# Kernel tuning notes

Measured on AMD Instinct MI355X. Metric: run time of the kernel, lower is better.

Reference implementation:

```python
import jax, jax.numpy as jnp
import numpy as np

B, L, H, E, F, C = 8, 8192, 512, 8, 1024, 2  # batch, seq, hidden, experts, ffn, capacity factor


def setup_inputs() -> dict:
    key = jax.random.key(0)
    ks = jax.random.split(key, 4)
    x = jax.random.normal(ks[0], (B, L, H), jnp.float32)
    Wg = jax.random.normal(ks[1], (H, E), jnp.float32) * (H ** -0.5)   # gate (no bias)
    W1 = jax.random.normal(ks[2], (E, H, F), jnp.float32) * (H ** -0.5)
    b1 = jnp.zeros((E, F), jnp.float32)
    W2 = jax.random.normal(ks[3], (E, F, H), jnp.float32) * (F ** -0.5)
    b2 = jnp.zeros((E, H), jnp.float32)
    return {"x": x, "Wg": Wg, "W1": W1, "b1": b1, "W2": W2, "b2": b2}


def reference(x, Wg, W1, b1, W2, b2):
    b, l, h = x.shape
    e = Wg.shape[1]
    k = min(max(int(l * C / e), 1), l)  # expert-choice capacity per expert
    # Gate scores: softmax over experts per token, then each expert picks its top-k tokens.
    S = jax.nn.softmax(x @ Wg, axis=-1)          # (b, l, E)
    St = jnp.swapaxes(S, 1, 2)                   # (b, E, l)
    G, I = jax.lax.top_k(St, k)                  # (b, E, k) scores / token indices
    # Dispatch: gather each expert's chosen tokens.
    ex = jnp.take_along_axis(x[:, None], I[..., None], axis=2)   # (b, E, k, h)
    # Grouped expert MLP (Linear -> GELU -> Linear), batched over experts.
    hmid = jax.nn.gelu(jnp.einsum('bekh,ehf->bekf', ex, W1) + b1[None, :, None, :],
                       approximate=False)
    out = jnp.einsum('bekf,efh->bekh', hmid, W2) + b2[None, :, None, :]
    vals = G[..., None] * out                    # weight by gate score
    # Combine: scatter-add expert outputs back to token positions.
    new_x = jnp.zeros_like(x).at[jnp.arange(b)[:, None, None], I].add(vals)
    return new_x
```

## Files before the change

kernel.cpp:

```cpp
#include <hip/hip_runtime.h>
#include <hip/hip_bf16.h>
#include <hip/hip_fp16.h>

typedef float f32x4 __attribute__((ext_vector_type(4)));
typedef _Float16 f16x8 __attribute__((ext_vector_type(8)));

static constexpr int Bb = 8, Ll = 8192, Hh = 512, Ee = 8, Ff = 1024, KK = 2048;

static __device__ __forceinline__ float fast_rcp(float x) {
#if __has_builtin(__builtin_amdgcn_rcpf)
  return __builtin_amdgcn_rcpf(x);
#else
  return 1.0f / x;
#endif
}

static __device__ __forceinline__ float gelu_exact(float v) {
  float a = __builtin_fabsf(v) * 0.70710678118654752f;
  float t = fast_rcp(__builtin_fmaf(0.3275911f, a, 1.0f));
  float p = __builtin_fmaf(1.061405429f, t, -1.453152027f);
  p = __builtin_fmaf(p, t, 1.421413741f);
  p = __builtin_fmaf(p, t, -0.284496736f);
  p = __builtin_fmaf(p, t, 0.254829592f);
  p = p * t;
  float e = __expf(-a * a);
  float er = __builtin_fmaf(-p, e, 1.0f);
  er = __builtin_copysignf(er, v);
  return 0.5f * v * (1.0f + er);
}

__global__ __launch_bounds__(256) void cvt_f16_kernel(const float* __restrict__ src,
                                                      _Float16* __restrict__ dst, int n4) {
  int i = blockIdx.x * blockDim.x + threadIdx.x;
  int stride = gridDim.x * blockDim.x;
  for (; i < n4; i += stride) {
    float4 v = reinterpret_cast<const float4*>(src)[i];
    union { _Float16 h[4]; uint2 u; } cv;
    cv.h[0] = (_Float16)v.x; cv.h[1] = (_Float16)v.y;
    cv.h[2] = (_Float16)v.z; cv.h[3] = (_Float16)v.w;
    reinterpret_cast<uint2*>(dst)[i] = cv.u;
  }
}

__global__ __launch_bounds__(256) void transpose_cvt_kernel(const float* __restrict__ src,
                                                            _Float16* __restrict__ dst,
                                                            int R, int C) {
  __shared__ float tile[32][33];
  int z = blockIdx.z;
  const float* s = src + (size_t)z * R * C;
  _Float16* d = dst + (size_t)z * R * C;
  int c0 = blockIdx.x * 32, r0 = blockIdx.y * 32;
  int tx = threadIdx.x, ty = threadIdx.y;
#pragma unroll
  for (int i = ty; i < 32; i += 8) tile[i][tx] = s[(size_t)(r0 + i) * C + (c0 + tx)];
  __syncthreads();
#pragma unroll
  for (int i = ty; i < 32; i += 8) d[(size_t)(c0 + i) * R + (r0 + tx)] = (_Float16)tile[tx][i];
}

__global__ __launch_bounds__(256) void gate_kernel(const float* __restrict__ x,
                                                   const float* __restrict__ Wg,
                                                   double* __restrict__ St) {
  __shared__ float wgt[8][516];
  __shared__ float xs[32][68];
  int tid = threadIdx.x;
  for (int i = tid; i < Hh * Ee; i += 256) {
    int h = i >> 3, e = i & 7;
    wgt[e][h] = Wg[i];
  }
  int tl = tid >> 3, e = tid & 7;
  int token0 = blockIdx.x * 32;
  double acc = 0.0;
  for (int c = 0; c < 8; ++c) {
    __syncthreads();
#pragma unroll
    for (int i = tid; i < 512; i += 256) {
      int row = i >> 4, c4 = i & 15;
      float4 v = reinterpret_cast<const float4*>(x + (size_t)(token0 + row) * Hh + c * 64)[c4];
      *reinterpret_cast<float4*>(&xs[row][c4 * 4]) = v;
    }
    __syncthreads();
#pragma unroll
    for (int h = 0; h < 64; h += 4) {
      float4 xv = *reinterpret_cast<const float4*>(&xs[tl][h]);
      float4 wv = *reinterpret_cast<const float4*>(&wgt[e][c * 64 + h]);
      acc += (double)xv.x * (double)wv.x;
      acc += (double)xv.y * (double)wv.y;
      acc += (double)xv.z * (double)wv.z;
      acc += (double)xv.w * (double)wv.w;
    }
  }
  double m = acc;
  m = fmax(m, __shfl_xor(m, 1, 64));
  m = fmax(m, __shfl_xor(m, 2, 64));
  m = fmax(m, __shfl_xor(m, 4, 64));
  double ex = exp(acc - m);
  double s = ex;
  s += __shfl_xor(s, 1, 64);
  s += __shfl_xor(s, 2, 64);
  s += __shfl_xor(s, 4, 64);
  int token = token0 + tl;
  int b = token >> 13, l = token & (Ll - 1);
  St[((size_t)(b * Ee + e)) * Ll + l] = ex / s;
}

__global__ __launch_bounds__(1024) void topk_kernel(const double* __restrict__ St,
                                                    int* __restrict__ idx,
                                                    float* __restrict__ gate) {
  __shared__ unsigned long long keys[Ll];
  __shared__ unsigned int hist[256];
  __shared__ unsigned int sc[1024];
  __shared__ unsigned long long s_prefix;
  __shared__ int s_remaining;
  __shared__ unsigned long long redA[16], redO[16];
  int row = blockIdx.x;
  int tid = threadIdx.x;
  const double* s = St + (size_t)row * Ll;
  unsigned long long myA = ~0ULL, myO = 0ULL;
  for (int i = tid; i < Ll; i += 1024) {
    unsigned long long kx = (unsigned long long)__double_as_longlong(s[i]);
    keys[i] = kx;
    myA &= kx;
    myO |= kx;
  }
#pragma unroll
  for (int off2 = 32; off2 >= 1; off2 >>= 1) {
    myA &= __shfl_xor(myA, off2, 64);
    myO |= __shfl_xor(myO, off2, 64);
  }
  if ((tid & 63) == 0) { redA[tid >> 6] = myA; redO[tid >> 6] = myO; }
  __syncthreads();
  unsigned long long allA = redA[0], allO = redO[0];
#pragma unroll
  for (int w = 1; w < 16; ++w) { allA &= redA[w]; allO |= redO[w]; }
  unsigned long long diff = allA ^ allO;

  unsigned long long T;
  int nEqTake;
  if (diff == 0) {
    T = allA;
    nEqTake = KK;
  } else {
    int hb = 63 - __builtin_clzll(diff);
    int pv = hb >> 3;
    unsigned long long prefmask = (pv >= 7) ? 0ULL : (~0ULL << ((pv + 1) * 8));
    unsigned long long prefix = allA & prefmask;
    int remaining = KK;
    for (int p = pv; p >= 0; --p) {
      if (tid < 256) hist[tid] = 0;
      __syncthreads();
      int sh = p * 8;
      for (int i = tid; i < Ll; i += 1024) {
        unsigned long long kk = keys[i];
        if ((kk & prefmask) == prefix) atomicAdd(&hist[(unsigned)(kk >> sh) & 255u], 1u);
      }
      __syncthreads();
      if (tid < 256) sc[tid] = hist[tid];
      __syncthreads();
#pragma unroll
      for (int off = 1; off < 256; off <<= 1) {
        unsigned v = (tid < 256 && tid + off < 256) ? sc[tid + off] : 0;
        __syncthreads();
        if (tid < 256) sc[tid] += v;
        __syncthreads();
      }
      if (tid < 256) {
        unsigned incl = sc[tid];
        unsigned above = (tid == 255) ? 0u : sc[tid + 1];
        if ((int)incl >= remaining && (int)above < remaining) {
          s_remaining = remaining - (int)above;
          s_prefix = prefix | ((unsigned long long)(unsigned)tid << sh);
        }
      }
      __syncthreads();
      remaining = s_remaining;
      prefix = s_prefix;
      prefmask |= (255ULL << sh);
      __syncthreads();
    }
    T = prefix;
    nEqTake = remaining;
  }

  int base = tid * 8;
  unsigned long long kk[8];
  unsigned gtc = 0, eqc = 0;
#pragma unroll
  for (int j = 0; j < 8; ++j) {
    kk[j] = keys[base + j];
    gtc += (kk[j] > T);
    eqc += (kk[j] == T);
  }
  unsigned packed = (gtc << 16) | eqc;
  sc[tid] = packed;
  __syncthreads();
  for (int off = 1; off < 1024; off <<= 1) {
    unsigned v = (tid >= off) ? sc[tid - off] : 0;
    __syncthreads();
    sc[tid] += v;
    __syncthreads();
  }
  unsigned excl = sc[tid] - packed;
  int gtb = (int)(excl >> 16), eqb = (int)(excl & 0xFFFFu);
  int orow = row * KK;
#pragma unroll
  for (int j = 0; j < 8; ++j) {
    bool isgt = kk[j] > T, iseq = kk[j] == T;
    bool take = isgt || (iseq && eqb < nEqTake);
    if (take) {
      int pos = gtb + (eqb < nEqTake ? eqb : nEqTake);
      idx[orow + pos] = base + j;
      gate[orow + pos] = (float)__longlong_as_double((long long)kk[j]);
    }
    gtb += isgt ? 1 : 0;
    eqb += iseq ? 1 : 0;
  }
}

__global__ __launch_bounds__(256) void buildinv_kernel(const int* __restrict__ idx,
                                                       int* __restrict__ cnt,
                                                       int* __restrict__ inv) {
  int s = blockIdx.x * 256 + threadIdx.x;
  int gp = s >> 11;
  int b = gp >> 3;
  int t = idx[s];
  int key = b * Ll + t;
  int pos = atomicAdd(&cnt[key], 1);
  inv[key * 8 + pos] = s;
}

__global__ __launch_bounds__(256) void combine_kernel(const _Float16* __restrict__ yout,
                                                      const int* __restrict__ cnt,
                                                      const int* __restrict__ inv,
                                                      float* __restrict__ out) {
  int tglob = blockIdx.x * 4 + (threadIdx.x >> 6);
  int lane = threadIdx.x & 63;
  int n = cnt[tglob];
  float acc[8];
#pragma unroll
  for (int j = 0; j < 8; ++j) acc[j] = 0.f;
  for (int c = 0; c < n; ++c) {
    int s = inv[tglob * 8 + c];
    f16x8 v = *reinterpret_cast<const f16x8*>(yout + (size_t)s * Hh + lane * 8);
#pragma unroll
    for (int j = 0; j < 8; ++j) acc[j] += (float)v[j];
  }
  float* o = out + (size_t)tglob * Hh + lane * 8;
  f32x4 lo = {acc[0], acc[1], acc[2], acc[3]};
  f32x4 hi = {acc[4], acc[5], acc[6], acc[7]};
  *reinterpret_cast<f32x4*>(o) = lo;
  *reinterpret_cast<f32x4*>(o + 4) = hi;
}

__global__ __launch_bounds__(512, 2) void gemm1_kernel(const _Float16* __restrict__ xb,
                                                       const _Float16* __restrict__ w1t,
                                                       const float* __restrict__ b1,
                                                       const int* __restrict__ idx,
                                                       _Float16* __restrict__ hmid,
                                                       int chunk_base) {
  __shared__ __align__(16) _Float16 lds[65536];
  int tid = threadIdx.x, lane = tid & 63, wid = tid >> 6;
  int gp = chunk_base + blockIdx.z;
  int b = gp >> 3, e = gp & 7;
  int m0 = blockIdx.y * 256, f0 = blockIdx.x * 256;

  const _Float16* srcbase[4];
  int dstoff[4];
#pragma unroll
  for (int i = 0; i < 4; ++i) {
    int c = wid * 4 + i;
    int lr = (c & 15) * 16 + (lane >> 2);
    int q = lane & 3;
    int qg = q ^ ((lr >> 1) & 3);
    if (c < 16) {
      int token = idx[(size_t)gp * KK + m0 + lr];
      srcbase[i] = xb + ((size_t)b * Ll + token) * Hh + qg * 8;
      dstoff[i] = (c & 15) * 512;
    } else {
      srcbase[i] = w1t + ((size_t)e * Ff + f0 + lr) * Hh + qg * 8;
      dstoff[i] = 8192 + (c & 15) * 512;
    }
  }

  f32x4 acc[8][4] = {};
  int wm = wid >> 2, wn = wid & 3;
  int a_off[8], b_off[4];
  int ko = lane >> 4;
#pragma unroll
  for (int i = 0; i < 8; ++i) {
    int ra = wm * 128 + i * 16 + (lane & 15);
    a_off[i] = ra * 32 + (ko ^ ((ra >> 1) & 3)) * 8;
  }
#pragma unroll
  for (int i = 0; i < 4; ++i) {
    int rb = wn * 64 + i * 16 + (lane & 15);
    b_off[i] = 8192 + rb * 32 + (ko ^ ((rb >> 1) & 3)) * 8;
  }

  auto stage = [&](int p, int kt) {
#pragma unroll
    for (int i = 0; i < 4; ++i) {
      __builtin_amdgcn_global_load_lds(
          (const __attribute__((address_space(1))) void*)(srcbase[i] + kt),
          (__attribute__((address_space(3))) void*)(lds + p * 16384 + dstoff[i]), 16, 0, 0);
    }
  };

  constexpr int nt = Hh / 32;
  stage(0, 0);
  stage(1, 32);
  for (int t = 0; t < nt; ++t) {
    __builtin_amdgcn_sched_barrier(0);
    if (t + 1 < nt) asm volatile("s_waitcnt vmcnt(4) lgkmcnt(0)" ::: "memory");
    else            asm volatile("s_waitcnt vmcnt(0) lgkmcnt(0)" ::: "memory");
    __builtin_amdgcn_s_barrier();
    __builtin_amdgcn_sched_barrier(0);
    if (t + 2 < nt) stage((t + 2) & 3, (t + 2) * 32);
    const _Float16* buf = lds + (t & 3) * 16384;
    f16x8 af[8], bf[4];
#pragma unroll
    for (int i = 0; i < 8; ++i) af[i] = *reinterpret_cast<const f16x8*>(buf + a_off[i]);
#pragma unroll
    for (int i = 0; i < 4; ++i) bf[i] = *reinterpret_cast<const f16x8*>(buf + b_off[i]);
    __builtin_amdgcn_s_setprio(1);
#pragma unroll
    for (int fr = 0; fr < 8; ++fr)
#pragma unroll
      for (int fc = 0; fc < 4; ++fc)
        acc[fr][fc] = __builtin_amdgcn_mfma_f32_16x16x32_f16(af[fr], bf[fc], acc[fr][fc], 0, 0, 0);
    __builtin_amdgcn_s_setprio(0);
  }
  __syncthreads();

  int cidx = lane & 15, rbase = (lane >> 4) * 4;
  float b1v[4];
#pragma unroll
  for (int fc = 0; fc < 4; ++fc) b1v[fc] = b1[e * Ff + f0 + wn * 64 + fc * 16 + cidx];
#pragma unroll
  for (int fr = 0; fr < 8; ++fr) {
#pragma unroll
    for (int fc = 0; fc < 4; ++fc) {
#pragma unroll
      for (int r = 0; r < 4; ++r) {
        int lm = wm * 128 + fr * 16 + rbase + r;
        int lf = wn * 64 + fc * 16 + cidx;
        float v = acc[fr][fc][r] + b1v[fc];
        float g = gelu_exact(v);
        lds[lm * 256 + (((lf >> 3) ^ (lm & 7)) << 3) + (lf & 7)] = (_Float16)g;
      }
    }
  }
  __syncthreads();
  _Float16* hd = hmid + (size_t)blockIdx.z * KK * Ff;
  int orow = tid >> 5, seg = tid & 31;
#pragma unroll
  for (int pp = 0; pp < 16; ++pp) {
    int lm = pp * 16 + orow;
    f16x8 v = *reinterpret_cast<const f16x8*>(lds + lm * 256 + ((seg ^ (lm & 7)) << 3));
    *reinterpret_cast<f16x8*>(hd + (size_t)(m0 + lm) * Ff + f0 + seg * 8) = v;
  }
}

__global__ __launch_bounds__(512, 2) void gemm2_kernel(const _Float16* __restrict__ hmid,
                                                       const _Float16* __restrict__ w2t,
                                                       const float* __restrict__ b2,
                                                       const int* __restrict__ idx,
                                                       const float* __restrict__ gate,
                                                       _Float16* __restrict__ yout,
                                                       int chunk_base) {
  __shared__ __align__(16) _Float16 lds[65536];
  int tid = threadIdx.x, lane = tid & 63, wid = tid >> 6;
  int gp = chunk_base + blockIdx.z;
  int e = gp & 7;
  int m0 = blockIdx.y * 256, h0 = blockIdx.x * 256;

  const _Float16* srcbase[4];
  int dstoff[4];
#pragma unroll
  for (int i = 0; i < 4; ++i) {
    int c = wid * 4 + i;
    int lr = (c & 15) * 16 + (lane >> 2);
    int q = lane & 3;
    int qg = q ^ ((lr >> 1) & 3);
    if (c < 16) {
      srcbase[i] = hmid + ((size_t)blockIdx.z * KK + m0 + lr) * Ff + qg * 8;
      dstoff[i] = (c & 15) * 512;
    } else {
      srcbase[i] = w2t + ((size_t)e * Hh + h0 + lr) * Ff + qg * 8;
      dstoff[i] = 8192 + (c & 15) * 512;
    }
  }

  f32x4 acc[8][4] = {};
  int wm = wid >> 2, wn = wid & 3;
  int a_off[8], b_off[4];
  int ko = lane >> 4;
#pragma unroll
  for (int i = 0; i < 8; ++i) {
    int ra = wm * 128 + i * 16 + (lane & 15);
    a_off[i] = ra * 32 + (ko ^ ((ra >> 1) & 3)) * 8;
  }
#pragma unroll
  for (int i = 0; i < 4; ++i) {
    int rb = wn * 64 + i * 16 + (lane & 15);
    b_off[i] = 8192 + rb * 32 + (ko ^ ((rb >> 1) & 3)) * 8;
  }

  auto stage = [&](int p, int kt) {
#pragma unroll
    for (int i = 0; i < 4; ++i) {
      __builtin_amdgcn_global_load_lds(
          (const __attribute__((address_space(1))) void*)(srcbase[i] + kt),
          (__attribute__((address_space(3))) void*)(lds + p * 16384 + dstoff[i]), 16, 0, 0);
    }
  };

  constexpr int nt = Ff / 32;
  stage(0, 0);
  stage(1, 32);
  for (int t = 0; t < nt; ++t) {
    __builtin_amdgcn_sched_barrier(0);
    if (t + 1 < nt) asm volatile("s_waitcnt vmcnt(4) lgkmcnt(0)" ::: "memory");
    else            asm volatile("s_waitcnt vmcnt(0) lgkmcnt(0)" ::: "memory");
    __builtin_amdgcn_s_barrier();
    __builtin_amdgcn_sched_barrier(0);
    if (t + 2 < nt) stage((t + 2) & 3, (t + 2) * 32);
    const _Float16* buf = lds + (t & 3) * 16384;
    f16x8 af[8], bf[4];
#pragma unroll
    for (int i = 0; i < 8; ++i) af[i] = *reinterpret_cast<const f16x8*>(buf + a_off[i]);
#pragma unroll
    for (int i = 0; i < 4; ++i) bf[i] = *reinterpret_cast<const f16x8*>(buf + b_off[i]);
    __builtin_amdgcn_s_setprio(1);
#pragma unroll
    for (int fr = 0; fr < 8; ++fr)
#pragma unroll
      for (int fc = 0; fc < 4; ++fc)
        acc[fr][fc] = __builtin_amdgcn_mfma_f32_16x16x32_f16(af[fr], bf[fc], acc[fr][fc], 0, 0, 0);
    __builtin_amdgcn_s_setprio(0);
  }
  __syncthreads();

  int cidx = lane & 15, rbase = (lane >> 4) * 4;
  float b2v[4];
#pragma unroll
  for (int fc = 0; fc < 4; ++fc) b2v[fc] = b2[e * Hh + h0 + wn * 64 + fc * 16 + cidx];
#pragma unroll
  for (int fr = 0; fr < 8; ++fr) {
    float gv[4];
#pragma unroll
    for (int r = 0; r < 4; ++r) {
      int lm = wm * 128 + fr * 16 + rbase + r;
      gv[r] = gate[(size_t)gp * KK + m0 + lm];
    }
#pragma unroll
    for (int fc = 0; fc < 4; ++fc) {
#pragma unroll
      for (int r = 0; r < 4; ++r) {
        int lm = wm * 128 + fr * 16 + rbase + r;
        int lh = wn * 64 + fc * 16 + cidx;
        float v = acc[fr][fc][r] + b2v[fc];
        lds[lm * 256 + (((lh >> 3) ^ (lm & 7)) << 3) + (lh & 7)] = (_Float16)(gv[r] * v);
      }
    }
  }
  __syncthreads();
  int orow = tid >> 5, seg = tid & 31;
#pragma unroll
  for (int pp = 0; pp < 16; ++pp) {
    int lm = pp * 16 + orow;
    f16x8 v = *reinterpret_cast<const f16x8*>(lds + lm * 256 + ((seg ^ (lm & 7)) << 3));
    *reinterpret_cast<f16x8*>(yout + ((size_t)gp * KK + m0 + lm) * Hh + h0 + seg * 8) = v;
  }
}

extern "C" void kernel_launch(void* const* d_in, const int* in_sizes, int n_in,
                              void* d_out, int out_size, void* d_ws, size_t ws_size,
                              hipStream_t stream) {
  const float* x  = (const float*)d_in[0];
  const float* Wg = (const float*)d_in[1];
  const float* W1 = (const float*)d_in[2];
  const float* b1 = (const float*)d_in[3];
  const float* W2 = (const float*)d_in[4];
  const float* b2 = (const float*)d_in[5];
  float* out = (float*)d_out;

  char* ws = (char*)d_ws;
  size_t off = 0;
  auto alloc = [&](size_t bytes) -> char* {
    char* p = ws + off;
    off = (off + bytes + 255) & ~(size_t)255;
    return p;
  };
  _Float16* xb   = (_Float16*)alloc((size_t)Bb * Ll * Hh * 2);
  _Float16* w1t  = (_Float16*)alloc((size_t)Ee * Ff * Hh * 2);
  _Float16* w2t  = (_Float16*)alloc((size_t)Ee * Hh * Ff * 2);
  double*   St   = (double*)alloc((size_t)Bb * Ee * Ll * 8);
  int*      dI   = (int*)alloc((size_t)Bb * Ee * KK * 4);
  float*    dG   = (float*)alloc((size_t)Bb * Ee * KK * 4);
  int*      cnt  = (int*)alloc((size_t)Bb * Ll * 4);
  int*      inv  = (int*)alloc((size_t)Bb * Ll * 8 * 4);
  _Float16* yout = (_Float16*)alloc((size_t)Bb * Ee * KK * Hh * 2);
  size_t fixed = off;
  size_t per_pair = (size_t)KK * Ff * 2;
  int chunk = 1;
  if (fixed + per_pair * 16 <= ws_size) chunk = 16;
  else if (fixed + per_pair * 8 <= ws_size) chunk = 8;
  else if (fixed + per_pair * 4 <= ws_size) chunk = 4;
  else if (fixed + per_pair * 2 <= ws_size) chunk = 2;
  _Float16* hmid = (_Float16*)alloc(per_pair * (size_t)chunk);

  hipMemsetAsync(cnt, 0, (size_t)Bb * Ll * 4, stream);
  cvt_f16_kernel<<<4096, 256, 0, stream>>>(x, xb, Bb * Ll * Hh / 4);
  transpose_cvt_kernel<<<dim3(Ff / 32, Hh / 32, Ee), dim3(32, 8), 0, stream>>>(W1, w1t, Hh, Ff);
  transpose_cvt_kernel<<<dim3(Hh / 32, Ff / 32, Ee), dim3(32, 8), 0, stream>>>(W2, w2t, Ff, Hh);
  gate_kernel<<<Bb * Ll / 32, 256, 0, stream>>>(x, Wg, St);
  topk_kernel<<<Bb * Ee, 1024, 0, stream>>>(St, dI, dG);
  buildinv_kernel<<<Bb * Ee * KK / 256, 256, 0, stream>>>(dI, cnt, inv);

  for (int cb = 0; cb < Bb * Ee; cb += chunk) {
    gemm1_kernel<<<dim3(Ff / 256, KK / 256, chunk), 512, 0, stream>>>(xb, w1t, b1, dI, hmid, cb);
    gemm2_kernel<<<dim3(Hh / 256, KK / 256, chunk), 512, 0, stream>>>(hmid, w2t, b2, dI, dG, yout, cb);
  }
  combine_kernel<<<Bb * Ll / 4, 256, 0, stream>>>(yout, cnt, inv, out);
}
```

Measured before the change: 591.4 us.

## Fuse x fp16 conversion into gate kernel; use BK=64 double-buffered GEMM pipeline

```diff
diff --git a/kernel.cpp b/kernel.cpp
--- a/kernel.cpp
+++ b/kernel.cpp
@@ -29,19 +29,6 @@
   return 0.5f * v * (1.0f + er);
 }
 
-__global__ __launch_bounds__(256) void cvt_f16_kernel(const float* __restrict__ src,
-                                                      _Float16* __restrict__ dst, int n4) {
-  int i = blockIdx.x * blockDim.x + threadIdx.x;
-  int stride = gridDim.x * blockDim.x;
-  for (; i < n4; i += stride) {
-    float4 v = reinterpret_cast<const float4*>(src)[i];
-    union { _Float16 h[4]; uint2 u; } cv;
-    cv.h[0] = (_Float16)v.x; cv.h[1] = (_Float16)v.y;
-    cv.h[2] = (_Float16)v.z; cv.h[3] = (_Float16)v.w;
-    reinterpret_cast<uint2*>(dst)[i] = cv.u;
-  }
-}
-
 __global__ __launch_bounds__(256) void transpose_cvt_kernel(const float* __restrict__ src,
                                                             _Float16* __restrict__ dst,
                                                             int R, int C) {
@@ -58,9 +45,10 @@
   for (int i = ty; i < 32; i += 8) d[(size_t)(c0 + i) * R + (r0 + tx)] = (_Float16)tile[tx][i];
 }
 
-__global__ __launch_bounds__(256) void gate_kernel(const float* __restrict__ x,
-                                                   const float* __restrict__ Wg,
-                                                   double* __restrict__ St) {
+__global__ __launch_bounds__(256) void gatecvt_kernel(const float* __restrict__ x,
+                                                      const float* __restrict__ Wg,
+                                                      double* __restrict__ St,
+                                                      _Float16* __restrict__ xb) {
   __shared__ float wgt[8][516];
   __shared__ float xs[32][68];
   int tid = threadIdx.x;
@@ -80,6 +68,15 @@
       *reinterpret_cast<float4*>(&xs[row][c4 * 4]) = v;
     }
     __syncthreads();
+    {
+      int row = tid >> 3, c8 = tid & 7;
+      float4 v0 = *reinterpret_cast<const float4*>(&xs[row][c8 * 8]);
+      float4 v1 = *reinterpret_cast<const float4*>(&xs[row][c8 * 8 + 4]);
+      f16x8 h;
+      h[0] = (_Float16)v0.x; h[1] = (_Float16)v0.y; h[2] = (_Float16)v0.z; h[3] = (_Float16)v0.w;
+      h[4] = (_Float16)v1.x; h[5] = (_Float16)v1.y; h[6] = (_Float16)v1.z; h[7] = (_Float16)v1.w;
+      *reinterpret_cast<f16x8*>(xb + (size_t)(token0 + row) * Hh + c * 64 + c8 * 8) = h;
+    }
 #pragma unroll
     for (int h = 0; h < 64; h += 4) {
       float4 xv = *reinterpret_cast<const float4*>(&xs[tl][h]);
@@ -264,21 +261,21 @@
   int b = gp >> 3, e = gp & 7;
   int m0 = blockIdx.y * 256, f0 = blockIdx.x * 256;
 
-  const _Float16* srcbase[4];
-  int dstoff[4];
-#pragma unroll
-  for (int i = 0; i < 4; ++i) {
-    int c = wid * 4 + i;
-    int lr = (c & 15) * 16 + (lane >> 2);
-    int q = lane & 3;
-    int qg = q ^ ((lr >> 1) & 3);
-    if (c < 16) {
+  const _Float16* srcbase[8];
+  int dstoff[8];
+#pragma unroll
+  for (int i = 0; i < 8; ++i) {
+    int c = wid * 8 + i;
+    int lr = (c & 31) * 8 + (lane >> 3);
+    int q = lane & 7;
+    int qg = q ^ (lr & 7);
+    if (c < 32) {
       int token = idx[(size_t)gp * KK + m0 + lr];
       srcbase[i] = xb + ((size_t)b * Ll + token) * Hh + qg * 8;
-      dstoff[i] = (c & 15) * 512;
+      dstoff[i] = (c & 31) * 512;
     } else {
       srcbase[i] = w1t + ((size_t)e * Ff + f0 + lr) * Hh + qg * 8;
-      dstoff[i] = 8192 + (c & 15) * 512;
+      dstoff[i] = 16384 + (c & 31) * 512;
     }
   }
 
@@ -289,46 +286,45 @@
 #pragma unroll
   for (int i = 0; i < 8; ++i) {
     int ra = wm * 128 + i * 16 + (lane & 15);
-    a_off[i] = ra * 32 + (ko ^ ((ra >> 1) & 3)) * 8;
+    a_off[i] = ra * 64 + (ko ^ (ra & 7)) * 8;
   }
 #pragma unroll
   for (int i = 0; i < 4; ++i) {
     int rb = wn * 64 + i * 16 + (lane & 15);
-    b_off[i] = 8192 + rb * 32 + (ko ^ ((rb >> 1) & 3)) * 8;
+    b_off[i] = 16384 + rb * 64 + (ko ^ (rb & 7)) * 8;
   }
 
   auto stage = [&](int p, int kt) {
 #pragma unroll
-    for (int i = 0; i < 4; ++i) {
+    for (int i = 0; i < 8; ++i) {
       __builtin_amdgcn_global_load_lds(
           (const __attribute__((address_space(1))) void*)(srcbase[i] + kt),
-          (__attribute__((address_space(3))) void*)(lds + p * 16384 + dstoff[i]), 16, 0, 0);
+          (__attribute__((address_space(3))) void*)(lds + p * 32768 + dstoff[i]), 16, 0, 0);
     }
   };
 
-  constexpr int nt = Hh / 32;
+  constexpr int nt = Hh / 64;
   stage(0, 0);
-  stage(1, 32);
   for (int t = 0; t < nt; ++t) {
-    __builtin_amdgcn_sched_barrier(0);
-    if (t + 1 < nt) asm volatile("s_waitcnt vmcnt(4) lgkmcnt(0)" ::: "memory");
-    else            asm volatile("s_waitcnt vmcnt(0) lgkmcnt(0)" ::: "memory");
-    __builtin_amdgcn_s_barrier();
-    __builtin_amdgcn_sched_barrier(0);
-    if (t + 2 < nt) stage((t + 2) & 3, (t + 2) * 32);
-    const _Float16* buf = lds + (t & 3) * 16384;
-    f16x8 af[8], bf[4];
-#pragma unroll
-    for (int i = 0; i < 8; ++i) af[i] = *reinterpret_cast<const f16x8*>(buf + a_off[i]);
-#pragma unroll
-    for (int i = 0; i < 4; ++i) bf[i] = *reinterpret_cast<const f16x8*>(buf + b_off[i]);
-    __builtin_amdgcn_s_setprio(1);
-#pragma unroll
-    for (int fr = 0; fr < 8; ++fr)
-#pragma unroll
-      for (int fc = 0; fc < 4; ++fc)
-        acc[fr][fc] = __builtin_amdgcn_mfma_f32_16x16x32_f16(af[fr], bf[fc], acc[fr][fc], 0, 0, 0);
-    __builtin_amdgcn_s_setprio(0);
+    __syncthreads();
+    if (t + 1 < nt) stage((t + 1) & 1, (t + 1) * 64);
+    const _Float16* buf = lds + (t & 1) * 32768;
+#pragma unroll
+    for (int half = 0; half < 2; ++half) {
+      int kx = half * 32;
+      f16x8 af[8], bf[4];
+#pragma unroll
+      for (int i = 0; i < 8; ++i) af[i] = *reinterpret_cast<const f16x8*>(buf + (a_off[i] ^ kx));
+#pragma unroll
+      for (int i = 0; i < 4; ++i) bf[i] = *reinterpret_cast<const f16x8*>(buf + (b_off[i] ^ kx));
+      __builtin_amdgcn_s_setprio(1);
+#pragma unroll
+      for (int fr = 0; fr < 8; ++fr)
+#pragma unroll
+        for (int fc = 0; fc < 4; ++fc)
+          acc[fr][fc] = __builtin_amdgcn_mfma_f32_16x16x32_f16(af[fr], bf[fc], acc[fr][fc], 0, 0, 0);
+      __builtin_amdgcn_s_setprio(0);
+    }
   }
   __syncthreads();
 
@@ -374,20 +370,20 @@
   int e = gp & 7;
   int m0 = blockIdx.y * 256, h0 = blockIdx.x * 256;
 
-  const _Float16* srcbase[4];
-  int dstoff[4];
-#pragma unroll
-  for (int i = 0; i < 4; ++i) {
-    int c = wid * 4 + i;
-    int lr = (c & 15) * 16 + (lane >> 2);
-    int q = lane & 3;
-    int qg = q ^ ((lr >> 1) & 3);
-    if (c < 16) {
+  const _Float16* srcbase[8];
+  int dstoff[8];
+#pragma unroll
+  for (int i = 0; i < 8; ++i) {
+    int c = wid * 8 + i;
+    int lr = (c & 31) * 8 + (lane >> 3);
+    int q = lane & 7;
+    int qg = q ^ (lr & 7);
+    if (c < 32) {
       srcbase[i] = hmid + ((size_t)blockIdx.z * KK + m0 + lr) * Ff + qg * 8;
-      dstoff[i] = (c & 15) * 512;
+      dstoff[i] = (c & 31) * 512;
     } else {
       srcbase[i] = w2t + ((size_t)e * Hh + h0 + lr) * Ff + qg * 8;
-      dstoff[i] = 8192 + (c & 15) * 512;
+      dstoff[i] = 16384 + (c & 31) * 512;
     }
   }
 
@@ -398,46 +394,45 @@
 #pragma unroll
   for (int i = 0; i < 8; ++i) {
     int ra = wm * 128 + i * 16 + (lane & 15);
-    a_off[i] = ra * 32 + (ko ^ ((ra >> 1) & 3)) * 8;
+    a_off[i] = ra * 64 + (ko ^ (ra & 7)) * 8;
   }
 #pragma unroll
   for (int i = 0; i < 4; ++i) {
     int rb = wn * 64 + i * 16 + (lane & 15);
-    b_off[i] = 8192 + rb * 32 + (ko ^ ((rb >> 1) & 3)) * 8;
+    b_off[i] = 16384 + rb * 64 + (ko ^ (rb & 7)) * 8;
   }
 
   auto stage = [&](int p, int kt) {
 #pragma unroll
-    for (int i = 0; i < 4; ++i) {
+    for (int i = 0; i < 8; ++i) {
       __builtin_amdgcn_global_load_lds(
           (const __attribute__((address_space(1))) void*)(srcbase[i] + kt),
-          (__attribute__((address_space(3))) void*)(lds + p * 16384 + dstoff[i]), 16, 0, 0);
+          (__attribute__((address_space(3))) void*)(lds + p * 32768 + dstoff[i]), 16, 0, 0);
     }
   };
 
-  constexpr int nt = Ff / 32;
+  constexpr int nt = Ff / 64;
   stage(0, 0);
-  stage(1, 32);
   for (int t = 0; t < nt; ++t) {
-    __builtin_amdgcn_sched_barrier(0);
-    if (t + 1 < nt) asm volatile("s_waitcnt vmcnt(4) lgkmcnt(0)" ::: "memory");
-    else            asm volatile("s_waitcnt vmcnt(0) lgkmcnt(0)" ::: "memory");
-    __builtin_amdgcn_s_barrier();
-    __builtin_amdgcn_sched_barrier(0);
-    if (t + 2 < nt) stage((t + 2) & 3, (t + 2) * 32);
-    const _Float16* buf = lds + (t & 3) * 16384;
-    f16x8 af[8], bf[4];
-#pragma unroll
-    for (int i = 0; i < 8; ++i) af[i] = *reinterpret_cast<const f16x8*>(buf + a_off[i]);
-#pragma unroll
-    for (int i = 0; i < 4; ++i) bf[i] = *reinterpret_cast<const f16x8*>(buf + b_off[i]);
-    __builtin_amdgcn_s_setprio(1);
-#pragma unroll
-    for (int fr = 0; fr < 8; ++fr)
-#pragma unroll
-      for (int fc = 0; fc < 4; ++fc)
-        acc[fr][fc] = __builtin_amdgcn_mfma_f32_16x16x32_f16(af[fr], bf[fc], acc[fr][fc], 0, 0, 0);
-    __builtin_amdgcn_s_setprio(0);
+    __syncthreads();
+    if (t + 1 < nt) stage((t + 1) & 1, (t + 1) * 64);
+    const _Float16* buf = lds + (t & 1) * 32768;
+#pragma unroll
+    for (int half = 0; half < 2; ++half) {
+      int kx = half * 32;
+      f16x8 af[8], bf[4];
+#pragma unroll
+      for (int i = 0; i < 8; ++i) af[i] = *reinterpret_cast<const f16x8*>(buf + (a_off[i] ^ kx));
+#pragma unroll
+      for (int i = 0; i < 4; ++i) bf[i] = *reinterpret_cast<const f16x8*>(buf + (b_off[i] ^ kx));
+      __builtin_amdgcn_s_setprio(1);
+#pragma unroll
+      for (int fr = 0; fr < 8; ++fr)
+#pragma unroll
+        for (int fc = 0; fc < 4; ++fc)
+          acc[fr][fc] = __builtin_amdgcn_mfma_f32_16x16x32_f16(af[fr], bf[fc], acc[fr][fc], 0, 0, 0);
+      __builtin_amdgcn_s_setprio(0);
+    }
   }
   __syncthreads();
 
@@ -511,10 +506,9 @@
   _Float16* hmid = (_Float16*)alloc(per_pair * (size_t)chunk);
 
   hipMemsetAsync(cnt, 0, (size_t)Bb * Ll * 4, stream);
-  cvt_f16_kernel<<<4096, 256, 0, stream>>>(x, xb, Bb * Ll * Hh / 4);
+  gatecvt_kernel<<<Bb * Ll / 32, 256, 0, stream>>>(x, Wg, St, xb);
   transpose_cvt_kernel<<<dim3(Ff / 32, Hh / 32, Ee), dim3(32, 8), 0, stream>>>(W1, w1t, Hh, Ff);
   transpose_cvt_kernel<<<dim3(Hh / 32, Ff / 32, Ee), dim3(32, 8), 0, stream>>>(W2, w2t, Ff, Hh);
-  gate_kernel<<<Bb * Ll / 32, 256, 0, stream>>>(x, Wg, St);
   topk_kernel<<<Bb * Ee, 1024, 0, stream>>>(St, dI, dG);
   buildinv_kernel<<<Bb * Ee * KK / 256, 256, 0, stream>>>(dI, cnt, inv);
 
```

Result: faster. 564.1 us (-4.6%).
